# Kernel tuning notes

Measured on AMD Instinct MI355X. Metric: run time of the kernel, lower is better.

Reference implementation:

```python
import jax, jax.numpy as jnp
import numpy as np

LAYERS, BLOCKS = 10, 4
NL = LAYERS * BLOCKS
RC, DC, SC, EC, CLASSES, K = 32, 32, 256, 256, 256, 2
B, T = 8, 16384


def setup_inputs() -> dict:
    key = jax.random.key(0)
    ks = jax.random.split(key, 10)
    s = 0.1  # small init so tanh/sigmoid stay in informative range
    f32 = jnp.float32
    return {
        "x": jax.random.normal(ks[0], (B, CLASSES, T), dtype=f32),
        "w_in": jax.random.normal(ks[1], (RC, CLASSES, 1), dtype=f32) * s,
        "b_in": jnp.zeros((RC,), dtype=f32),
        "filt_w": jax.random.normal(ks[2], (NL, DC, RC, K), dtype=f32) * s,
        "filt_b": jnp.zeros((NL, DC), dtype=f32),
        "gate_w": jax.random.normal(ks[3], (NL, DC, RC, K), dtype=f32) * s,
        "gate_b": jnp.zeros((NL, DC), dtype=f32),
        "res_w": jax.random.normal(ks[4], (NL, RC, DC, K), dtype=f32) * s,
        "res_b": jnp.zeros((NL, RC), dtype=f32),
        "skip_w": jax.random.normal(ks[5], (NL, SC, DC, K), dtype=f32) * s,
        "skip_b": jnp.zeros((NL, SC), dtype=f32),
        "end1_w": jax.random.normal(ks[6], (EC, SC, 1), dtype=f32) * s,
        "end1_b": jnp.zeros((EC,), dtype=f32),
        "end2_w": jax.random.normal(ks[7], (CLASSES, EC, 1), dtype=f32) * s,
        "end2_b": jnp.zeros((CLASSES,), dtype=f32),
    }


def _causal_conv(x, w, b, d):
    # Equivalent to torch Conv1d(padding=d, dilation=d, k=2) followed by [:, :, :L]:
    # y[t] = w[..,0] @ x[t-d] + w[..,1] @ x[t]
    y = jax.lax.conv_general_dilated(
        x, w, window_strides=(1,), padding=[(d, 0)], rhs_dilation=(d,),
        dimension_numbers=("NCH", "OIH", "NCH"))
    return y + b[None, :, None]


def _conv1x1(x, w, b):
    return jnp.einsum("bct,oc->bot", x, w[:, :, 0]) + b[None, :, None]


def reference(x, w_in, b_in, filt_w, filt_b, gate_w, gate_b,
              res_w, res_b, skip_w, skip_b, end1_w, end1_b, end2_w, end2_b):
    h = _conv1x1(x, w_in, b_in)                      # [B, RC, T]
    skip = jnp.zeros((x.shape[0], SC, x.shape[2]), dtype=x.dtype)
    for i in range(NL):
        d = 2 ** (i % LAYERS)
        f = jnp.tanh(_causal_conv(h, filt_w[i], filt_b[i], d))
        g = jax.nn.sigmoid(_causal_conv(h, gate_w[i], gate_b[i], d))
        z = f * g                                    # [B, DC, T]
        skip = skip + _causal_conv(z, skip_w[i], skip_b[i], d)
        h = h + _causal_conv(z, res_w[i], res_b[i], d)
    out = jax.nn.relu(skip)
    out = jax.nn.relu(_conv1x1(out, end1_w, end1_b))
    out = _conv1x1(out, end2_w, end2_b)              # [B, CLASSES, T]
    n, c, l = out.shape
    return out.transpose(0, 2, 1).reshape(n * l, c)  # [B*T, CLASSES]
```

## Files before the change

kernel.cpp:

```cpp
#include <hip/hip_runtime.h>
#include <cstdint>
#include <cstddef>

#define T_LEN    16384
#define BATCH    8
#define BT       (BATCH * T_LEN)
#define NLAYERS  40

typedef unsigned short ushort_t;
typedef unsigned int   uint_t;
typedef __attribute__((ext_vector_type(8))) short    short8;
typedef __attribute__((ext_vector_type(4))) float    float4v;
typedef __attribute__((ext_vector_type(8))) _Float16 half8;

__device__ __forceinline__ ushort_t f2bf(float f) {
    union { float f; uint_t i; } v; v.f = f;
    uint_t r = (v.i + 0x7FFFu + ((v.i >> 16) & 1u)) >> 16;
    return (ushort_t)r;
}
__device__ __forceinline__ float fast_rcp(float x) {
#if __has_builtin(__builtin_amdgcn_rcpf)
    return __builtin_amdgcn_rcpf(x);
#else
    return 1.f / x;
#endif
}
__device__ __forceinline__ float tanh_fast(float x) {
    float e = __expf(2.f * x);
    return 1.f - 2.f * fast_rcp(e + 1.f);
}
__device__ __forceinline__ float sigmoid_fast(float x) {
    return fast_rcp(1.f + __expf(-x));
}
__device__ __forceinline__ float4v mfma16(short8 a, short8 b, float4v c) {
    return __builtin_amdgcn_mfma_f32_16x16x32_bf16(a, b, c, 0, 0, 0);
}

__global__ __launch_bounds__(256) void k_prep(
    const float* __restrict__ filt_w, const float* __restrict__ gate_w,
    const float* __restrict__ res_w,  const float* __restrict__ skip_w,
    const float* __restrict__ end1_w, const float* __restrict__ end2_w,
    const float* __restrict__ filt_b, const float* __restrict__ gate_b,
    const float* __restrict__ res_b,  const float* __restrict__ skip_b,
    const float* __restrict__ end1_b, const float* __restrict__ end2_b,
    ushort_t* __restrict__ wfgF, ushort_t* __restrict__ wrF,
    ushort_t* __restrict__ bsF,  ushort_t* __restrict__ e1F, ushort_t* __restrict__ e2F,
    float* __restrict__ bfg, float* __restrict__ brb, float* __restrict__ bsum,
    float* __restrict__ b1,  float* __restrict__ b2)
{
    const int gt = blockIdx.x * blockDim.x + threadIdx.x;
    const int gs = gridDim.x * blockDim.x;

    for (int e = gt; e < NLAYERS * 4 * 2 * 512; e += gs) {
        int j = e & 7, lane = (e >> 3) & 63, f = e >> 9;
        int ks = f & 1, nt = (f >> 1) & 3, i = f >> 3;
        int ln = lane & 15, q = lane >> 4, c = q * 8 + j;
        int o = (nt & 1) * 16 + ln;
        float v = (nt < 2) ? filt_w[((i * 32 + o) * 32 + c) * 2 + ks]
                           : gate_w[((i * 32 + o) * 32 + c) * 2 + ks];
        wfgF[e] = f2bf(v);
    }
    for (int e = gt; e < NLAYERS * 2 * 2 * 512; e += gs) {
        int j = e & 7, lane = (e >> 3) & 63, f = e >> 9;
        int ks = f & 1, nt = (f >> 1) & 1, i = f >> 2;
        int ln = lane & 15, q = lane >> 4, c = q * 8 + j;
        int o = nt * 16 + ln;
        wrF[e] = f2bf(res_w[((i * 32 + o) * 32 + c) * 2 + ks]);
    }
    for (int e = gt; e < 80 * 16 * 512; e += gs) {
        int j = e & 7, lane = (e >> 3) & 63, f = e >> 9;
        int nt = f & 15, ks80 = f >> 4;
        int i = ks80 >> 1, tap = ks80 & 1;
        int ln = lane & 15, q = lane >> 4, c = q * 8 + j;
        int o = nt * 16 + ln;
        bsF[e] = f2bf(skip_w[((i * 256 + o) * 32 + c) * 2 + tap]);
    }
    for (int e = gt; e < 8 * 16 * 512; e += gs) {
        int j = e & 7, lane = (e >> 3) & 63, f = e >> 9;
        int nt = f & 15, ks = f >> 4;
        int ln = lane & 15, q = lane >> 4;
        int k = ks * 32 + q * 8 + j;
        int o = nt * 16 + ln;
        e1F[e] = f2bf(end1_w[o * 256 + k]);
        e2F[e] = f2bf(end2_w[o * 256 + k]);
    }
    for (int e = gt; e < NLAYERS * 64; e += gs) {
        int i = e >> 6, c = e & 63;
        bfg[e] = (c < 32) ? filt_b[i * 32 + c] : gate_b[i * 32 + (c - 32)];
    }
    for (int e = gt; e < NLAYERS * 32; e += gs) {
        int i = e >> 5, c = e & 31;
        brb[e] = res_b[i * 32 + c];
    }
    for (int e = gt; e < 256; e += gs) {
        float s = 0.f;
        for (int i = 0; i < NLAYERS; ++i) s += skip_b[i * 256 + e];
        bsum[e] = s;
        b1[e] = end1_b[e];
        b2[e] = end2_b[e];
    }
}

__global__ __launch_bounds__(256) void k_input(
    const float* __restrict__ x, const float* __restrict__ w_in,
    const float* __restrict__ b_in, _Float16* __restrict__ h16)
{
    __shared__ __align__(16) float ws[256 * 32];
    for (int idx = threadIdx.x; idx < 256 * 32; idx += 256) {
        int o = idx >> 8, c = idx & 255;
        ws[c * 32 + o] = w_in[idx];
    }
    __syncthreads();
    const int bt = blockIdx.x * 256 + threadIdx.x;
    const float* xp = x + (size_t)(bt >> 14) * 256 * T_LEN + (bt & (T_LEN - 1));
    float acc[32];
#pragma unroll
    for (int o = 0; o < 32; ++o) acc[o] = b_in[o];
    for (int c = 0; c < 256; ++c) {
        float xv = xp[(size_t)c * T_LEN];
        const float4v* wr = (const float4v*)&ws[c * 32];
#pragma unroll
        for (int g = 0; g < 8; ++g) {
            float4v w4 = wr[g];
            acc[g * 4 + 0] += xv * w4[0];
            acc[g * 4 + 1] += xv * w4[1];
            acc[g * 4 + 2] += xv * w4[2];
            acc[g * 4 + 3] += xv * w4[3];
        }
    }
    half8* dst = (half8*)(h16 + (size_t)bt * 32);
#pragma unroll
    for (int g = 0; g < 4; ++g) {
        half8 v;
#pragma unroll
        for (int j = 0; j < 8; ++j) v[j] = (_Float16)acc[g * 8 + j];
        dst[g] = v;
    }
}

__global__ __launch_bounds__(256) void k_fg(
    const _Float16* __restrict__ h16, const ushort_t* __restrict__ wfgF,
    const float* __restrict__ bfg, ushort_t* __restrict__ zAll,
    int layer, int dil)
{
    const int w = threadIdx.x >> 6, lane = threadIdx.x & 63;
    const int ln = lane & 15, q = lane >> 4;
    const int bt0 = (blockIdx.x * 4 + w) * 16;
    const int m = bt0 + ln;
    const int koff = q * 8;

    short8 a0 = {0, 0, 0, 0, 0, 0, 0, 0}, a1;
    {
        half8 hv = *(const half8*)(h16 + (size_t)m * 32 + koff);
#pragma unroll
        for (int j = 0; j < 8; ++j) a1[j] = (short)f2bf((float)hv[j]);
    }
    if ((m & (T_LEN - 1)) >= dil) {
        half8 hv = *(const half8*)(h16 + (size_t)(m - dil) * 32 + koff);
#pragma unroll
        for (int j = 0; j < 8; ++j) a0[j] = (short)f2bf((float)hv[j]);
    }

    const short8* wf8 = (const short8*)wfgF;
    const float4v vzero = {0.f, 0.f, 0.f, 0.f};
    float4v acc[4];
#pragma unroll
    for (int nt = 0; nt < 4; ++nt) {
        float4v c = vzero;
        short8 b0 = wf8[(((size_t)layer * 4 + nt) * 2 + 0) * 64 + lane];
        short8 b1 = wf8[(((size_t)layer * 4 + nt) * 2 + 1) * 64 + lane];
        c = mfma16(a0, b0, c);
        c = mfma16(a1, b1, c);
        acc[nt] = c;
    }

    const float bF0 = bfg[layer * 64 + ln],      bF1 = bfg[layer * 64 + 16 + ln];
    const float bG0 = bfg[layer * 64 + 32 + ln], bG1 = bfg[layer * 64 + 48 + ln];
    ushort_t* zl = zAll + (size_t)layer * BT * 32;
#pragma unroll
    for (int r = 0; r < 4; ++r) {
        int row = bt0 + q * 4 + r;
        float z0 = tanh_fast(acc[0][r] + bF0) * sigmoid_fast(acc[2][r] + bG0);
        float z1 = tanh_fast(acc[1][r] + bF1) * sigmoid_fast(acc[3][r] + bG1);
        zl[(size_t)row * 32 + ln]      = f2bf(z0);
        zl[(size_t)row * 32 + 16 + ln] = f2bf(z1);
    }
}

__global__ __launch_bounds__(256) void k_resfg(
    const _Float16* __restrict__ hin, _Float16* __restrict__ hout,
    ushort_t* __restrict__ zAll,
    const ushort_t* __restrict__ wrF, const float* __restrict__ brb,
    const ushort_t* __restrict__ wfgF, const float* __restrict__ bfg,
    int layer, int dil, int dilN)
{
    __shared__ float lds[4][2][2][16 * 33];
    const int w = threadIdx.x >> 6, lane = threadIdx.x & 63;
    const int ln = lane & 15, q = lane >> 4;
    const int koff = q * 8;
    const int bt0 = (blockIdx.x * 4 + w) * 32;
    const ushort_t* zl = zAll + (size_t)layer * BT * 32;
    ushort_t* zo = zAll + (size_t)(layer + 1) * BT * 32;
    const short8* wr8 = (const short8*)wrF;
    const short8* wf8 = (const short8*)wfgF;
    const float4v vzero = {0.f, 0.f, 0.f, 0.f};
    const short8 zero8 = {0, 0, 0, 0, 0, 0, 0, 0};

    const short8 rb00 = wr8[(((size_t)layer * 2 + 0) * 2 + 0) * 64 + lane];
    const short8 rb01 = wr8[(((size_t)layer * 2 + 0) * 2 + 1) * 64 + lane];
    const short8 rb10 = wr8[(((size_t)layer * 2 + 1) * 2 + 0) * 64 + lane];
    const short8 rb11 = wr8[(((size_t)layer * 2 + 1) * 2 + 1) * 64 + lane];
    const float br0 = brb[layer * 32 + ln], br1 = brb[layer * 32 + 16 + ln];

#pragma unroll
    for (int mt = 0; mt < 2; ++mt) {
        const int mb = bt0 + mt * 16;
        const int m = mb + ln;
        const int tln = m & (T_LEN - 1);
        short8 a1 = *(const short8*)(zl + (size_t)m * 32 + koff);
        short8 a0 = (tln >= dil) ? *(const short8*)(zl + (size_t)(m - dil) * 32 + koff) : zero8;
        float4v c0 = mfma16(a0, rb00, vzero); c0 = mfma16(a1, rb01, c0);
        float4v c1 = mfma16(a0, rb10, vzero); c1 = mfma16(a1, rb11, c1);
        short8 p1 = (tln >= dilN)       ? *(const short8*)(zl + (size_t)(m - dilN) * 32 + koff)       : zero8;
        short8 p0 = (tln >= dilN + dil) ? *(const short8*)(zl + (size_t)(m - dilN - dil) * 32 + koff) : zero8;
        float4v d0 = mfma16(p0, rb00, vzero); d0 = mfma16(p1, rb01, d0);
        float4v d1 = mfma16(p0, rb10, vzero); d1 = mfma16(p1, rb11, d1);

        float* t0 = &lds[w][mt][0][0];
        float* t1 = &lds[w][mt][1][0];
#pragma unroll
        for (int r = 0; r < 4; ++r) {
            int row = q * 4 + r;
            int grow = mb + row;
            int tr = grow & (T_LEN - 1);
            float h0a = (float)hin[(size_t)grow * 32 + ln];
            float h0b = (float)hin[(size_t)grow * 32 + 16 + ln];
            t0[row * 33 + ln]      = c0[r] + br0 + h0a;
            t0[row * 33 + 16 + ln] = c1[r] + br1 + h0b;
            float hpa = 0.f, hpb = 0.f;
            if (tr >= dilN) {
                hpa = (float)hin[(size_t)(grow - dilN) * 32 + ln]      + d0[r] + br0;
                hpb = (float)hin[(size_t)(grow - dilN) * 32 + 16 + ln] + d1[r] + br1;
            }
            t1[row * 33 + ln]      = hpa;
            t1[row * 33 + 16 + ln] = hpb;
        }
    }
    __syncthreads();

    const int L1 = layer + 1;
    const float bF0 = bfg[L1 * 64 + ln],      bF1 = bfg[L1 * 64 + 16 + ln];
    const float bG0 = bfg[L1 * 64 + 32 + ln], bG1 = bfg[L1 * 64 + 48 + ln];
#pragma unroll
    for (int mt = 0; mt < 2; ++mt) {
        const int mb = bt0 + mt * 16;
        const float* t0 = &lds[w][mt][0][0];
        const float* t1 = &lds[w][mt][1][0];
        short8 fa1, fa0;
#pragma unroll
        for (int j = 0; j < 8; ++j) {
            fa1[j] = (short)f2bf(t0[ln * 33 + koff + j]);
            fa0[j] = (short)f2bf(t1[ln * 33 + koff + j]);
        }
        float4v acc[4];
#pragma unroll
        for (int nt = 0; nt < 4; ++nt) {
            float4v c = vzero;
            c = mfma16(fa0, wf8[(((size_t)L1 * 4 + nt) * 2 + 0) * 64 + lane], c);
            c = mfma16(fa1, wf8[(((size_t)L1 * 4 + nt) * 2 + 1) * 64 + lane], c);
            acc[nt] = c;
        }
#pragma unroll
        for (int r = 0; r < 4; ++r) {
            int row = mb + q * 4 + r;
            float z0 = tanh_fast(acc[0][r] + bF0) * sigmoid_fast(acc[2][r] + bG0);
            float z1 = tanh_fast(acc[1][r] + bF1) * sigmoid_fast(acc[3][r] + bG1);
            zo[(size_t)row * 32 + ln]      = f2bf(z0);
            zo[(size_t)row * 32 + 16 + ln] = f2bf(z1);
        }
        half8 hv;
#pragma unroll
        for (int j = 0; j < 8; ++j) hv[j] = (_Float16)t0[ln * 33 + q * 8 + j];
        *(half8*)(hout + (size_t)(mb + ln) * 32 + q * 8) = hv;
    }
}

__global__ __launch_bounds__(512) void k_skip_gemm(
    const ushort_t* __restrict__ zAll, const ushort_t* __restrict__ bsF,
    const float* __restrict__ bsum, ushort_t* __restrict__ skipbuf)
{
    __shared__ __align__(16) ushort_t ldsB[32 * 512];
    const int tid = threadIdx.x;
    const int w = tid >> 6, lane = tid & 63;
    const int wR = w >> 2, wC = w & 3;
    const int ln = lane & 15, q = lane >> 4, koff = q * 8;
    const int mBase = blockIdx.x * 128 + wR * 64;

    const float4v vzero = {0.f, 0.f, 0.f, 0.f};
    const short8 zero8 = {0, 0, 0, 0, 0, 0, 0, 0};
    float4v acc[4][4];
#pragma unroll
    for (int mt = 0; mt < 4; ++mt)
#pragma unroll
        for (int nt = 0; nt < 4; ++nt) acc[mt][nt] = vzero;

    short8* lb = (short8*)ldsB;
    for (int i = 0; i < NLAYERS; ++i) {
        const short8* gsrc = (const short8*)(bsF + (size_t)i * 32 * 512);
        short8 s0 = gsrc[tid], s1 = gsrc[tid + 512], s2 = gsrc[tid + 1024], s3 = gsrc[tid + 1536];

        const int dil = 1 << (i % 10);
        const ushort_t* zl = zAll + (size_t)i * BT * 32;
        short8 a1[4], a0[4];
#pragma unroll
        for (int mt = 0; mt < 4; ++mt) {
            int m = mBase + mt * 16 + ln;
            int tln = m & (T_LEN - 1);
            a1[mt] = *(const short8*)(zl + (size_t)m * 32 + koff);
            a0[mt] = (tln >= dil) ? *(const short8*)(zl + (size_t)(m - dil) * 32 + koff) : zero8;
        }
        lb[tid] = s0; lb[tid + 512] = s1; lb[tid + 1024] = s2; lb[tid + 1536] = s3;
        __syncthreads();
        short8 b0[4], b1[4];
#pragma unroll
        for (int nt = 0; nt < 4; ++nt) {
            b0[nt] = lb[(wC * 4 + nt) * 64 + lane];
            b1[nt] = lb[(16 + wC * 4 + nt) * 64 + lane];
        }
#pragma unroll
        for (int mt = 0; mt < 4; ++mt)
#pragma unroll
            for (int nt = 0; nt < 4; ++nt) {
                acc[mt][nt] = mfma16(a0[mt], b0[nt], acc[mt][nt]);
                acc[mt][nt] = mfma16(a1[mt], b1[nt], acc[mt][nt]);
            }
        __syncthreads();
    }

#pragma unroll
    for (int nt = 0; nt < 4; ++nt) {
        const int n = wC * 64 + nt * 16 + ln;
        const float bias = bsum[n];
#pragma unroll
        for (int mt = 0; mt < 4; ++mt)
#pragma unroll
            for (int r = 0; r < 4; ++r) {
                int row = mBase + mt * 16 + q * 4 + r;
                float v = fmaxf(acc[mt][nt][r] + bias, 0.f);
                skipbuf[(size_t)row * 256 + n] = f2bf(v);
            }
    }
}

__global__ __launch_bounds__(512) void k_end(
    const ushort_t* __restrict__ skipbuf, const ushort_t* __restrict__ e1F,
    const ushort_t* __restrict__ e2F, const float* __restrict__ b1,
    const float* __restrict__ b2, float* __restrict__ out)
{
    __shared__ __align__(16) ushort_t ldsS[16 * 512];
    __shared__ __align__(16) ushort_t ldsA[64 * 512];
    const int tid = threadIdx.x;
    const int w = tid >> 6, lane = tid & 63;
    const int wR = w >> 2, wC = w & 3;
    const int ln = lane & 15, q = lane >> 4, koff = q * 8;
    const int mBase = blockIdx.x * 128 + wR * 64;

    const float4v vzero = {0.f, 0.f, 0.f, 0.f};
    float4v acc[4][4];
#pragma unroll
    for (int mt = 0; mt < 4; ++mt)
#pragma unroll
        for (int nt = 0; nt < 4; ++nt) acc[mt][nt] = vzero;

    short8* ls = (short8*)ldsS;
    for (int ks = 0; ks < 8; ++ks) {
        const short8* gsrc = (const short8*)(e1F + (size_t)ks * 16 * 512);
        short8 s0 = gsrc[tid], s1 = gsrc[tid + 512];
        short8 a[4];
#pragma unroll
        for (int mt = 0; mt < 4; ++mt) {
            int m = mBase + mt * 16 + ln;
            a[mt] = *(const short8*)(skipbuf + (size_t)m * 256 + ks * 32 + koff);
        }
        ls[tid] = s0; ls[tid + 512] = s1;
        __syncthreads();
        short8 bfr[4];
#pragma unroll
        for (int nt = 0; nt < 4; ++nt) bfr[nt] = ls[(wC * 4 + nt) * 64 + lane];
#pragma unroll
        for (int mt = 0; mt < 4; ++mt)
#pragma unroll
            for (int nt = 0; nt < 4; ++nt)
                acc[mt][nt] = mfma16(a[mt], bfr[nt], acc[mt][nt]);
        __syncthreads();
    }
#pragma unroll
    for (int nt = 0; nt < 4; ++nt) {
        const int col = wC * 64 + nt * 16 + ln;
        const float bb = b1[col];
        const int fk = col >> 5;
        const int l2hi = ((col >> 3) & 3) << 4;
        const int j = col & 7;
#pragma unroll
        for (int mt = 0; mt < 4; ++mt) {
            const int fr = wR * 4 + mt;
#pragma unroll
            for (int r = 0; r < 4; ++r) {
                int lane2 = (q * 4 + r) | l2hi;
                float v = fmaxf(acc[mt][nt][r] + bb, 0.f);
                ldsA[((fr * 8 + fk) * 64 + lane2) * 8 + j] = f2bf(v);
            }
        }
    }
    __syncthreads();
#pragma unroll
    for (int mt = 0; mt < 4; ++mt)
#pragma unroll
        for (int nt = 0; nt < 4; ++nt) acc[mt][nt] = vzero;
    for (int ks = 0; ks < 8; ++ks) {
        const short8* gsrc = (const short8*)(e2F + (size_t)ks * 16 * 512);
        short8 s0 = gsrc[tid], s1 = gsrc[tid + 512];
        short8 a[4];
#pragma unroll
        for (int mt = 0; mt < 4; ++mt)
            a[mt] = ((const short8*)ldsA)[((size_t)(wR * 4 + mt) * 8 + ks) * 64 + lane];
        ls[tid] = s0; ls[tid + 512] = s1;
        __syncthreads();
        short8 bfr[4];
#pragma unroll
        for (int nt = 0; nt < 4; ++nt) bfr[nt] = ls[(wC * 4 + nt) * 64 + lane];
#pragma unroll
        for (int mt = 0; mt < 4; ++mt)
#pragma unroll
            for (int nt = 0; nt < 4; ++nt)
                acc[mt][nt] = mfma16(a[mt], bfr[nt], acc[mt][nt]);
        __syncthreads();
    }
#pragma unroll
    for (int nt = 0; nt < 4; ++nt) {
        const int n = wC * 64 + nt * 16 + ln;
        const float bb = b2[n];
#pragma unroll
        for (int mt = 0; mt < 4; ++mt)
#pragma unroll
            for (int r = 0; r < 4; ++r) {
                int row = mBase + mt * 16 + q * 4 + r;
                out[(size_t)row * 256 + n] = acc[mt][nt][r] + bb;
            }
    }
}

extern "C" void kernel_launch(void* const* d_in, const int* in_sizes, int n_in,
                              void* d_out, int out_size, void* d_ws, size_t ws_size,
                              hipStream_t stream)
{
    (void)in_sizes; (void)n_in; (void)out_size; (void)ws_size;
    const float* x      = (const float*)d_in[0];
    const float* w_in   = (const float*)d_in[1];
    const float* b_in   = (const float*)d_in[2];
    const float* filt_w = (const float*)d_in[3];
    const float* filt_b = (const float*)d_in[4];
    const float* gate_w = (const float*)d_in[5];
    const float* gate_b = (const float*)d_in[6];
    const float* res_w  = (const float*)d_in[7];
    const float* res_b  = (const float*)d_in[8];
    const float* skip_w = (const float*)d_in[9];
    const float* skip_b = (const float*)d_in[10];
    const float* end1_w = (const float*)d_in[11];
    const float* end1_b = (const float*)d_in[12];
    const float* end2_w = (const float*)d_in[13];
    const float* end2_b = (const float*)d_in[14];

    char* ws = (char*)d_ws;
    size_t off = 0;
    auto alloc = [&](size_t bytes) {
        char* p = ws + off;
        off += (bytes + 255) & ~(size_t)255;
        return p;
    };
    ushort_t* zAll    = (ushort_t*)alloc((size_t)NLAYERS * BT * 32 * 2);
    ushort_t* skipbuf = (ushort_t*)alloc((size_t)BT * 256 * 2);
    _Float16* hA      = (_Float16*)skipbuf;
    _Float16* hB      = (_Float16*)(skipbuf + (size_t)BT * 32);
    ushort_t* wfgF    = (ushort_t*)alloc((size_t)NLAYERS * 4 * 2 * 512 * 2);
    ushort_t* wrF     = (ushort_t*)alloc((size_t)NLAYERS * 2 * 2 * 512 * 2);
    ushort_t* bsF     = (ushort_t*)alloc((size_t)80 * 16 * 512 * 2);
    ushort_t* e1F     = (ushort_t*)alloc((size_t)8 * 16 * 512 * 2);
    ushort_t* e2F     = (ushort_t*)alloc((size_t)8 * 16 * 512 * 2);
    float* bfg  = (float*)alloc((size_t)NLAYERS * 64 * 4);
    float* brb  = (float*)alloc((size_t)NLAYERS * 32 * 4);
    float* bsum = (float*)alloc(256 * 4);
    float* b1   = (float*)alloc(256 * 4);
    float* b2   = (float*)alloc(256 * 4);

    k_prep<<<256, 256, 0, stream>>>(filt_w, gate_w, res_w, skip_w, end1_w, end2_w,
                                    filt_b, gate_b, res_b, skip_b, end1_b, end2_b,
                                    wfgF, wrF, bsF, e1F, e2F, bfg, brb, bsum, b1, b2);
    k_input<<<BT / 256, 256, 0, stream>>>(x, w_in, b_in, hA);
    k_fg<<<BT / 64, 256, 0, stream>>>(hA, wfgF, bfg, zAll, 0, 1);
    for (int i = 0; i < NLAYERS - 1; ++i) {
        const _Float16* hin = (i & 1) ? hB : hA;
        _Float16*       ho  = (i & 1) ? hA : hB;
        int dil  = 1 << (i % 10);
        int dilN = 1 << ((i + 1) % 10);
        k_resfg<<<BT / 128, 256, 0, stream>>>(hin, ho, zAll, wrF, brb, wfgF, bfg,
                                              i, dil, dilN);
    }
    k_skip_gemm<<<BT / 128, 512, 0, stream>>>(zAll, bsF, bsum, skipbuf);
    k_end<<<BT / 128, 512, 0, stream>>>(skipbuf, e1F, e2F, b1, b2, (float*)d_out);
}
```

Before: 1.252 ms.

## Pipeline skip GEMM loads, drop LDS weight staging, hoist weights in resfg

k_skip_gemm now double-buffers the z and weight fragments in registers across layer pairs and reads the weights straight from global memory instead of staging them through LDS with barriers. It also swizzles the block index and requests two blocks per CU. k_end likewise drops LDS staging and its barriers for the end1/end2 weights. k_resfg hoists the next-layer weights and biases, loads h as vectors, shrinks the LDS tile and processes each m-tile in turn. The aim is to hide memory latency and cut syncs, at the cost of higher register pressure and more redundant global weight reads.

New measurement: 1.095 ms. -12.5%, faster.

```diff
diff --git a/kernel.cpp b/kernel.cpp
--- a/kernel.cpp
+++ b/kernel.cpp
@@ -194,7 +194,7 @@
     const ushort_t* __restrict__ wfgF, const float* __restrict__ bfg,
     int layer, int dil, int dilN)
 {
-    __shared__ float lds[4][2][2][16 * 33];
+    __shared__ __align__(16) float lds[4][2][16 * 36];
     const int w = threadIdx.x >> 6, lane = threadIdx.x & 63;
     const int ln = lane & 15, q = lane >> 4;
     const int koff = q * 8;
@@ -212,6 +212,19 @@
     const short8 rb11 = wr8[(((size_t)layer * 2 + 1) * 2 + 1) * 64 + lane];
     const float br0 = brb[layer * 32 + ln], br1 = brb[layer * 32 + 16 + ln];
 
+    const int L1 = layer + 1;
+    short8 fb0[4], fb1[4];
+#pragma unroll
+    for (int nt = 0; nt < 4; ++nt) {
+        fb0[nt] = wf8[(((size_t)L1 * 4 + nt) * 2 + 0) * 64 + lane];
+        fb1[nt] = wf8[(((size_t)L1 * 4 + nt) * 2 + 1) * 64 + lane];
+    }
+    const float bF0 = bfg[L1 * 64 + ln],      bF1 = bfg[L1 * 64 + 16 + ln];
+    const float bG0 = bfg[L1 * 64 + 32 + ln], bG1 = bfg[L1 * 64 + 48 + ln];
+
+    float* t0 = &lds[w][0][0];
+    float* t1 = &lds[w][1][0];
+
 #pragma unroll
     for (int mt = 0; mt < 2; ++mt) {
         const int mb = bt0 + mt * 16;
@@ -219,56 +232,46 @@
         const int tln = m & (T_LEN - 1);
         short8 a1 = *(const short8*)(zl + (size_t)m * 32 + koff);
         short8 a0 = (tln >= dil) ? *(const short8*)(zl + (size_t)(m - dil) * 32 + koff) : zero8;
+        short8 p1 = (tln >= dilN)       ? *(const short8*)(zl + (size_t)(m - dilN) * 32 + koff)       : zero8;
+        short8 p0 = (tln >= dilN + dil) ? *(const short8*)(zl + (size_t)(m - dilN - dil) * 32 + koff) : zero8;
+        const bool vld = (tln >= dilN);
+        half8 hv1 = *(const half8*)(hin + (size_t)m * 32 + koff);
+        half8 hv0 = {0, 0, 0, 0, 0, 0, 0, 0};
+        if (vld) hv0 = *(const half8*)(hin + (size_t)(m - dilN) * 32 + koff);
+
         float4v c0 = mfma16(a0, rb00, vzero); c0 = mfma16(a1, rb01, c0);
         float4v c1 = mfma16(a0, rb10, vzero); c1 = mfma16(a1, rb11, c1);
-        short8 p1 = (tln >= dilN)       ? *(const short8*)(zl + (size_t)(m - dilN) * 32 + koff)       : zero8;
-        short8 p0 = (tln >= dilN + dil) ? *(const short8*)(zl + (size_t)(m - dilN - dil) * 32 + koff) : zero8;
         float4v d0 = mfma16(p0, rb00, vzero); d0 = mfma16(p1, rb01, d0);
         float4v d1 = mfma16(p0, rb10, vzero); d1 = mfma16(p1, rb11, d1);
 
-        float* t0 = &lds[w][mt][0][0];
-        float* t1 = &lds[w][mt][1][0];
+        if (mt) __syncthreads();
 #pragma unroll
         for (int r = 0; r < 4; ++r) {
             int row = q * 4 + r;
-            int grow = mb + row;
-            int tr = grow & (T_LEN - 1);
-            float h0a = (float)hin[(size_t)grow * 32 + ln];
-            float h0b = (float)hin[(size_t)grow * 32 + 16 + ln];
-            t0[row * 33 + ln]      = c0[r] + br0 + h0a;
-            t0[row * 33 + 16 + ln] = c1[r] + br1 + h0b;
-            float hpa = 0.f, hpb = 0.f;
-            if (tr >= dilN) {
-                hpa = (float)hin[(size_t)(grow - dilN) * 32 + ln]      + d0[r] + br0;
-                hpb = (float)hin[(size_t)(grow - dilN) * 32 + 16 + ln] + d1[r] + br1;
-            }
-            t1[row * 33 + ln]      = hpa;
-            t1[row * 33 + 16 + ln] = hpb;
-        }
-    }
-    __syncthreads();
-
-    const int L1 = layer + 1;
-    const float bF0 = bfg[L1 * 64 + ln],      bF1 = bfg[L1 * 64 + 16 + ln];
-    const float bG0 = bfg[L1 * 64 + 32 + ln], bG1 = bfg[L1 * 64 + 48 + ln];
-#pragma unroll
-    for (int mt = 0; mt < 2; ++mt) {
-        const int mb = bt0 + mt * 16;
-        const float* t0 = &lds[w][mt][0][0];
-        const float* t1 = &lds[w][mt][1][0];
+            t0[row * 36 + ln]      = c0[r] + br0;
+            t0[row * 36 + 16 + ln] = c1[r] + br1;
+            t1[row * 36 + ln]      = d0[r] + br0;
+            t1[row * 36 + 16 + ln] = d1[r] + br1;
+        }
+        __syncthreads();
+
         short8 fa1, fa0;
+        half8 hw;
 #pragma unroll
         for (int j = 0; j < 8; ++j) {
-            fa1[j] = (short)f2bf(t0[ln * 33 + koff + j]);
-            fa0[j] = (short)f2bf(t1[ln * 33 + koff + j]);
-        }
+            float v1 = t0[ln * 36 + koff + j] + (float)hv1[j];
+            fa1[j] = (short)f2bf(v1);
+            hw[j]  = (_Float16)v1;
+            float v0 = vld ? (t1[ln * 36 + koff + j] + (float)hv0[j]) : 0.f;
+            fa0[j] = (short)f2bf(v0);
+        }
+        *(half8*)(hout + (size_t)m * 32 + koff) = hw;
+
         float4v acc[4];
 #pragma unroll
         for (int nt = 0; nt < 4; ++nt) {
-            float4v c = vzero;
-            c = mfma16(fa0, wf8[(((size_t)L1 * 4 + nt) * 2 + 0) * 64 + lane], c);
-            c = mfma16(fa1, wf8[(((size_t)L1 * 4 + nt) * 2 + 1) * 64 + lane], c);
-            acc[nt] = c;
+            float4v c = mfma16(fa0, fb0[nt], vzero);
+            acc[nt] = mfma16(fa1, fb1[nt], c);
         }
 #pragma unroll
         for (int r = 0; r < 4; ++r) {
@@ -278,63 +281,68 @@
             zo[(size_t)row * 32 + ln]      = f2bf(z0);
             zo[(size_t)row * 32 + 16 + ln] = f2bf(z1);
         }
-        half8 hv;
-#pragma unroll
-        for (int j = 0; j < 8; ++j) hv[j] = (_Float16)t0[ln * 33 + q * 8 + j];
-        *(half8*)(hout + (size_t)(mb + ln) * 32 + q * 8) = hv;
-    }
-}
-
-__global__ __launch_bounds__(512) void k_skip_gemm(
+    }
+}
+
+#define SG_LOAD(i, A0, A1, B0, B1) do {                                          \
+    const int dil_ = 1 << ((i) % 10);                                            \
+    const ushort_t* zl_ = zAll + (size_t)(i) * BT * 32;                          \
+    _Pragma("unroll")                                                            \
+    for (int mt_ = 0; mt_ < 4; ++mt_) {                                          \
+        int m_ = mBase + mt_ * 16 + ln;                                          \
+        int tln_ = m_ & (T_LEN - 1);                                             \
+        A1[mt_] = *(const short8*)(zl_ + (size_t)m_ * 32 + koff);                \
+        A0[mt_] = (tln_ >= dil_)                                                 \
+                ? *(const short8*)(zl_ + (size_t)(m_ - dil_) * 32 + koff)        \
+                : zero8;                                                         \
+    }                                                                            \
+    _Pragma("unroll")                                                            \
+    for (int nt_ = 0; nt_ < 4; ++nt_) {                                          \
+        B0[nt_] = bsrc[((size_t)((i) * 2 + 0) * 16 + wC * 4 + nt_) * 64 + lane]; \
+        B1[nt_] = bsrc[((size_t)((i) * 2 + 1) * 16 + wC * 4 + nt_) * 64 + lane]; \
+    }                                                                            \
+} while (0)
+
+#define SG_MMA(A0, A1, B0, B1) do {                                              \
+    _Pragma("unroll")                                                            \
+    for (int mt_ = 0; mt_ < 4; ++mt_)                                            \
+        _Pragma("unroll")                                                        \
+        for (int nt_ = 0; nt_ < 4; ++nt_) {                                      \
+            acc[mt_][nt_] = mfma16(A0[mt_], B0[nt_], acc[mt_][nt_]);             \
+            acc[mt_][nt_] = mfma16(A1[mt_], B1[nt_], acc[mt_][nt_]);             \
+        }                                                                        \
+} while (0)
+
+__global__ __launch_bounds__(512, 2) void k_skip_gemm(
     const ushort_t* __restrict__ zAll, const ushort_t* __restrict__ bsF,
     const float* __restrict__ bsum, ushort_t* __restrict__ skipbuf)
 {
-    __shared__ __align__(16) ushort_t ldsB[32 * 512];
     const int tid = threadIdx.x;
     const int w = tid >> 6, lane = tid & 63;
     const int wR = w >> 2, wC = w & 3;
     const int ln = lane & 15, q = lane >> 4, koff = q * 8;
-    const int mBase = blockIdx.x * 128 + wR * 64;
+    const int bid = blockIdx.x;
+    const int bsw = (bid & 7) * ((int)gridDim.x >> 3) + (bid >> 3);
+    const int mBase = bsw * 128 + wR * 64;
 
     const float4v vzero = {0.f, 0.f, 0.f, 0.f};
     const short8 zero8 = {0, 0, 0, 0, 0, 0, 0, 0};
+    const short8* bsrc = (const short8*)bsF;
     float4v acc[4][4];
 #pragma unroll
     for (int mt = 0; mt < 4; ++mt)
 #pragma unroll
         for (int nt = 0; nt < 4; ++nt) acc[mt][nt] = vzero;
 
-    short8* lb = (short8*)ldsB;
-    for (int i = 0; i < NLAYERS; ++i) {
-        const short8* gsrc = (const short8*)(bsF + (size_t)i * 32 * 512);
-        short8 s0 = gsrc[tid], s1 = gsrc[tid + 512], s2 = gsrc[tid + 1024], s3 = gsrc[tid + 1536];
-
-        const int dil = 1 << (i % 10);
-        const ushort_t* zl = zAll + (size_t)i * BT * 32;
-        short8 a1[4], a0[4];
-#pragma unroll
-        for (int mt = 0; mt < 4; ++mt) {
-            int m = mBase + mt * 16 + ln;
-            int tln = m & (T_LEN - 1);
-            a1[mt] = *(const short8*)(zl + (size_t)m * 32 + koff);
-            a0[mt] = (tln >= dil) ? *(const short8*)(zl + (size_t)(m - dil) * 32 + koff) : zero8;
-        }
-        lb[tid] = s0; lb[tid + 512] = s1; lb[tid + 1024] = s2; lb[tid + 1536] = s3;
-        __syncthreads();
-        short8 b0[4], b1[4];
-#pragma unroll
-        for (int nt = 0; nt < 4; ++nt) {
-            b0[nt] = lb[(wC * 4 + nt) * 64 + lane];
-            b1[nt] = lb[(16 + wC * 4 + nt) * 64 + lane];
-        }
-#pragma unroll
-        for (int mt = 0; mt < 4; ++mt)
-#pragma unroll
-            for (int nt = 0; nt < 4; ++nt) {
-                acc[mt][nt] = mfma16(a0[mt], b0[nt], acc[mt][nt]);
-                acc[mt][nt] = mfma16(a1[mt], b1[nt], acc[mt][nt]);
-            }
-        __syncthreads();
+    short8 xa0[4], xa1[4], xb0[4], xb1[4];
+    short8 ya0[4], ya1[4], yb0[4], yb1[4];
+    SG_LOAD(0, xa0, xa1, xb0, xb1);
+#pragma unroll 2
+    for (int i = 0; i < NLAYERS; i += 2) {
+        SG_LOAD(i + 1, ya0, ya1, yb0, yb1);
+        SG_MMA(xa0, xa1, xb0, xb1);
+        if (i + 2 < NLAYERS) SG_LOAD(i + 2, xa0, xa1, xb0, xb1);
+        SG_MMA(ya0, ya1, yb0, yb1);
     }
 
 #pragma unroll
@@ -357,7 +365,6 @@
     const ushort_t* __restrict__ e2F, const float* __restrict__ b1,
     const float* __restrict__ b2, float* __restrict__ out)
 {
-    __shared__ __align__(16) ushort_t ldsS[16 * 512];
     __shared__ __align__(16) ushort_t ldsA[64 * 512];
     const int tid = threadIdx.x;
     const int w = tid >> 6, lane = tid & 63;
@@ -365,6 +372,8 @@
     const int ln = lane & 15, q = lane >> 4, koff = q * 8;
     const int mBase = blockIdx.x * 128 + wR * 64;
 
+    const short8* e1s = (const short8*)e1F;
+    const short8* e2s = (const short8*)e2F;
     const float4v vzero = {0.f, 0.f, 0.f, 0.f};
     float4v acc[4][4];
 #pragma unroll
@@ -372,27 +381,22 @@
 #pragma unroll
         for (int nt = 0; nt < 4; ++nt) acc[mt][nt] = vzero;
 
-    short8* ls = (short8*)ldsS;
+#pragma unroll 2
     for (int ks = 0; ks < 8; ++ks) {
-        const short8* gsrc = (const short8*)(e1F + (size_t)ks * 16 * 512);
-        short8 s0 = gsrc[tid], s1 = gsrc[tid + 512];
-        short8 a[4];
+        short8 a[4], bfr[4];
 #pragma unroll
         for (int mt = 0; mt < 4; ++mt) {
             int m = mBase + mt * 16 + ln;
             a[mt] = *(const short8*)(skipbuf + (size_t)m * 256 + ks * 32 + koff);
         }
-        ls[tid] = s0; ls[tid + 512] = s1;
-        __syncthreads();
-        short8 bfr[4];
-#pragma unroll
-        for (int nt = 0; nt < 4; ++nt) bfr[nt] = ls[(wC * 4 + nt) * 64 + lane];
+#pragma unroll
+        for (int nt = 0; nt < 4; ++nt)
+            bfr[nt] = e1s[((size_t)ks * 16 + wC * 4 + nt) * 64 + lane];
 #pragma unroll
         for (int mt = 0; mt < 4; ++mt)
 #pragma unroll
             for (int nt = 0; nt < 4; ++nt)
                 acc[mt][nt] = mfma16(a[mt], bfr[nt], acc[mt][nt]);
-        __syncthreads();
     }
 #pragma unroll
     for (int nt = 0; nt < 4; ++nt) {
@@ -417,24 +421,20 @@
     for (int mt = 0; mt < 4; ++mt)
 #pragma unroll
         for (int nt = 0; nt < 4; ++nt) acc[mt][nt] = vzero;
+#pragma unroll 2
     for (int ks = 0; ks < 8; ++ks) {
-        const short8* gsrc = (const short8*)(e2F + (size_t)ks * 16 * 512);
-        short8 s0 = gsrc[tid], s1 = gsrc[tid + 512];
-        short8 a[4];
+        short8 a[4], bfr[4];
 #pragma unroll
         for (int mt = 0; mt < 4; ++mt)
             a[mt] = ((const short8*)ldsA)[((size_t)(wR * 4 + mt) * 8 + ks) * 64 + lane];
-        ls[tid] = s0; ls[tid + 512] = s1;
-        __syncthreads();
-        short8 bfr[4];
-#pragma unroll
-        for (int nt = 0; nt < 4; ++nt) bfr[nt] = ls[(wC * 4 + nt) * 64 + lane];
+#pragma unroll
+        for (int nt = 0; nt < 4; ++nt)
+            bfr[nt] = e2s[((size_t)ks * 16 + wC * 4 + nt) * 64 + lane];
 #pragma unroll
         for (int mt = 0; mt < 4; ++mt)
 #pragma unroll
             for (int nt = 0; nt < 4; ++nt)
                 acc[mt][nt] = mfma16(a[mt], bfr[nt], acc[mt][nt]);
-        __syncthreads();
     }
 #pragma unroll
     for (int nt = 0; nt < 4; ++nt) {
```
